# Kernel tuning notes

Hardware: AMD Instinct MI355X
Metric: run time of the kernel (lower is better)

## Reference

```python
import jax, jax.numpy as jnp
import numpy as np

GROUPS = 32
EPS = 1e-6


def group_norm(x, gamma, beta):
    # x: [B, C, T], normalize per group of channels over (C//G, T)
    B, C, T = x.shape
    xr = x.reshape(B, GROUPS, C // GROUPS, T)
    mean = xr.mean(axis=(2, 3), keepdims=True)
    var = xr.var(axis=(2, 3), keepdims=True)
    xn = ((xr - mean) * jax.lax.rsqrt(var + EPS)).reshape(B, C, T)
    return xn * gamma[None, :, None] + beta[None, :, None]


def conv1x1(h, w, b):
    # 1x1 Conv1d == channel matmul. h: [B,C,T], w: [O,C], b: [O]
    return jnp.einsum('oc,bct->bot', w, h) + b[None, :, None]


def setup_inputs() -> dict:
    key = jax.random.key(0)
    ks = jax.random.split(key, 10)
    B, C, T = 8, 512, 2048
    s = 1.0 / np.sqrt(C)
    return {
        'x': jax.random.normal(ks[0], (B, C, T), jnp.float32),
        'gamma': jnp.ones((C,), jnp.float32),
        'beta': jnp.zeros((C,), jnp.float32),
        'q_w': jax.random.normal(ks[1], (C, C), jnp.float32) * s,
        'q_b': jnp.zeros((C,), jnp.float32),
        'k_w': jax.random.normal(ks[2], (C, C), jnp.float32) * s,
        'k_b': jnp.zeros((C,), jnp.float32),
        'v_w': jax.random.normal(ks[3], (C, C), jnp.float32) * s,
        'v_b': jnp.zeros((C,), jnp.float32),
        'o_w': jax.random.normal(ks[4], (C, C), jnp.float32) * s,
        'o_b': jnp.zeros((C,), jnp.float32),
    }


def reference(x, gamma, beta, q_w, q_b, k_w, k_b, v_w, v_b, o_w, o_b):
    h = group_norm(x, gamma, beta)
    q = conv1x1(h, q_w, q_b)  # [B,C,T]
    k = conv1x1(h, k_w, k_b)
    v = conv1x1(h, v_w, v_b)
    B, C, T = q.shape
    scale = jnp.asarray(C, q.dtype) ** -0.5
    # scores[b,t,s] = sum_c q[b,c,t] * k[b,c,s]
    scores = jnp.einsum('bct,bcs->bts', q, k) * scale
    w = jax.nn.softmax(scores, axis=-1)
    # out[b,c,t] = sum_s v[b,c,s] * w[b,t,s]
    h = jnp.einsum('bcs,bts->bct', v, w)
    h = conv1x1(h, o_w, o_b)
    return x + h
```

## Files before the change

kernel.cpp:

```cpp
#include <hip/hip_runtime.h>
#include <hip/hip_bf16.h>
#include <stdint.h>

typedef __bf16 bf16_t;
typedef __attribute__((ext_vector_type(8))) __bf16 bf16x8;
typedef __attribute__((ext_vector_type(4))) __bf16 bf16x4;
typedef __attribute__((ext_vector_type(4))) float f32x4;

__device__ __forceinline__ bool is_fp32(const void* gamma) {
  return ((const unsigned*)gamma)[0] == 0x3F800000u;
}

__device__ __forceinline__ void async_copy16(const bf16_t* g, bf16_t* l) {
  __builtin_amdgcn_global_load_lds(
      (const __attribute__((address_space(1))) void*)g,
      (__attribute__((address_space(3))) void*)l, 16, 0, 0);
}

#define GFENCE() asm volatile("" ::: "memory")

__device__ __forceinline__ void hard_barrier() {
  GFENCE();
  __builtin_amdgcn_sched_barrier(0);
  __builtin_amdgcn_s_barrier();
  __builtin_amdgcn_sched_barrier(0);
  GFENCE();
}

template <int NW>
__device__ __forceinline__ void vm_wait() {
  if constexpr (NW == 8)
    asm volatile("s_waitcnt vmcnt(8)" ::: "memory");
  else if constexpr (NW == 6)
    asm volatile("s_waitcnt vmcnt(6)" ::: "memory");
  else if constexpr (NW == 3)
    asm volatile("s_waitcnt vmcnt(3)" ::: "memory");
  else
    asm volatile("s_waitcnt vmcnt(0)" ::: "memory");
}

__global__ __launch_bounds__(512) void gnorm(
    const void* __restrict__ xv, const void* __restrict__ gamma,
    const void* __restrict__ beta, const void* __restrict__ q_w,
    const void* __restrict__ k_w, const void* __restrict__ v_w,
    const void* __restrict__ o_w, const void* __restrict__ q_b,
    const void* __restrict__ k_b, const void* __restrict__ v_b,
    const void* __restrict__ o_b, bf16_t* __restrict__ wdst,
    float* __restrict__ rowsum, bf16_t* __restrict__ ht) {
  const bool fp32 = is_fp32(gamma);
  const int bid = blockIdx.x;
  const int tid = threadIdx.x;
  if (bid < 64) {
    const void* wsrc[4] = {q_w, k_w, v_w, o_w};
#pragma unroll
    for (int r = 0; r < 4; ++r) {
      int e = (bid * 2048 + r * 512 + tid) * 8;
      int seg = e >> 18, off = e & 262143;
      const void* s = wsrc[seg];
      bf16x8 w8;
      if (fp32) {
        const float* sf = (const float*)s + off;
        float4 u = *(const float4*)sf;
        float4 w = *(const float4*)(sf + 4);
        w8[0] = (bf16_t)u.x; w8[1] = (bf16_t)u.y;
        w8[2] = (bf16_t)u.z; w8[3] = (bf16_t)u.w;
        w8[4] = (bf16_t)w.x; w8[5] = (bf16_t)w.y;
        w8[6] = (bf16_t)w.z; w8[7] = (bf16_t)w.w;
      } else {
        w8 = *(const bf16x8*)((const bf16_t*)s + off);
      }
      *(bf16x8*)(wdst + e) = w8;
    }
    if (bid == 0) {
      bf16_t* vdst = wdst + 4 * 262144;
      const void* vsrc[6] = {gamma, beta, q_b, k_b, v_b, o_b};
#pragma unroll
      for (int rep = 0; rep < 6; ++rep) {
        const void* s2 = vsrc[rep];
        vdst[rep * 512 + tid] = fp32 ? (bf16_t)((const float*)s2)[tid]
                                     : ((const bf16_t*)s2)[tid];
      }
    }
    if (bid >= 1 && bid <= 8) {
      float4 z = {0.f, 0.f, 0.f, 0.f};
      *(float4*)(rowsum + (((bid - 1) << 9) + tid) * 4) = z;
    }
    return;
  }
  __shared__ float tile[16 * 2052];
  __shared__ float red[16];
  const int gn = bid - 64;
  const int b = gn >> 5, g = gn & 31;
  const long long base = ((long long)b * 512 + g * 16) * 2048;
  float s1 = 0.f, s2 = 0.f;
  if (fp32) {
    const float* xf = (const float*)xv + base;
#pragma unroll
    for (int p = 0; p < 16; ++p) {
      float4 u = *(const float4*)(xf + p * 2048 + tid * 4);
      s1 += u.x + u.y + u.z + u.w;
      s2 += u.x * u.x + u.y * u.y + u.z * u.z + u.w * u.w;
      *(float4*)&tile[p * 2052 + tid * 4] = u;
    }
  } else {
    const bf16_t* xb = (const bf16_t*)xv + base;
#pragma unroll
    for (int p = 0; p < 16; ++p) {
      bf16x4 v4 = *(const bf16x4*)(xb + p * 2048 + tid * 4);
      float4 u;
      u.x = (float)v4[0]; u.y = (float)v4[1];
      u.z = (float)v4[2]; u.w = (float)v4[3];
      s1 += u.x + u.y + u.z + u.w;
      s2 += u.x * u.x + u.y * u.y + u.z * u.z + u.w * u.w;
      *(float4*)&tile[p * 2052 + tid * 4] = u;
    }
  }
  for (int o = 32; o > 0; o >>= 1) {
    s1 += __shfl_down(s1, o);
    s2 += __shfl_down(s2, o);
  }
  const int wv = tid >> 6, ln = tid & 63;
  if (ln == 0) { red[wv] = s1; red[8 + wv] = s2; }
  __syncthreads();
  float a = 0.f, c2 = 0.f;
#pragma unroll
  for (int w = 0; w < 8; ++w) { a += red[w]; c2 += red[8 + w]; }
  const float inv = 1.0f / 32768.0f;
  float mean = a * inv;
  float var = c2 * inv - mean * mean;
  float rstd = rsqrtf(var + 1e-6f);

  const int c = ln & 15;
  const int tq = ln >> 4;
  const int gc = g * 16 + c;
  float gamv = fp32 ? ((const float*)gamma)[gc]
                    : (float)((const bf16_t*)gamma)[gc];
  float betv = fp32 ? ((const float*)beta)[gc]
                    : (float)((const bf16_t*)beta)[gc];
  float sc = rstd * gamv;
  float sh = betv - mean * sc;
  bf16_t* hb = ht + (long long)b * 2048 * 512 + g * 16;
#pragma unroll 4
  for (int pass = 0; pass < 64; ++pass) {
    int t = wv * 256 + pass * 4 + tq;
    float v = tile[c * 2052 + t];
    hb[(long long)t * 512 + c] = (bf16_t)(v * sc + sh);
  }
}

template <bool BIASM, bool BIASN, bool EXPSUM, int M, int N, int K, int LDA,
          int LDB, int LDC>
__device__ __forceinline__ void gemm_ring3(
    const bf16_t* __restrict__ A, long long sA, const bf16_t* __restrict__ B,
    long long sB, bf16_t* __restrict__ Cout, long long sC,
    const bf16_t* __restrict__ biasM, const bf16_t* __restrict__ biasN,
    float alpha, float* __restrict__ rowsum, int m0, int n0, int b,
    bf16_t* lds) {
  const int tid = threadIdx.x;
  const int lane = tid & 63;
  const int lane15 = lane & 15;
  const int quad = lane >> 4;
  const int wave = tid >> 6;
  const int wm = wave >> 2;
  const int wn = wave & 3;

  bf16_t* ldsA = lds;
  bf16_t* ldsB = lds + 3 * 4096;

  const int srow = tid >> 2;
  const int sg = ((tid & 3) - (srow >> 1)) & 3;
  const long long B128 = 128LL * LDB;
  const bf16_t* As_src = A + (long long)b * sA + (long long)m0 * LDA +
                         (long long)srow * LDA + sg * 8;
  const bf16_t* Bs_src = B + (long long)b * sB + (long long)n0 * LDB +
                         (long long)srow * LDB + sg * 8;

  auto stA = [&](int kelem, int r) {
    async_copy16(As_src + kelem, ldsA + r * 4096 + tid * 8);
  };
  auto stB = [&](int kelem, int r) {
    async_copy16(Bs_src + kelem, ldsB + r * 8192 + tid * 8);
    async_copy16(Bs_src + B128 + kelem, ldsB + r * 8192 + tid * 8 + 4096);
  };

  const int slot = ((quad + (lane15 >> 1)) & 3) * 8;
  const int aoff = (wm * 64 + lane15) * 32 + slot;
  const int boff = (wn * 64 + lane15) * 32 + slot;

  bf16x8 af[4];
  f32x4 acc[4][4];
#pragma unroll
  for (int i = 0; i < 4; ++i)
#pragma unroll
    for (int j = 0; j < 4; ++j) acc[i][j] = {0.f, 0.f, 0.f, 0.f};

  auto ldbf = [&](int r, int j) {
    return *(const bf16x8*)(ldsB + r * 8192 + boff + j * 512);
  };

  constexpr int NT = K / 32;

  stA(0, 0); stB(0, 0);
  stA(32, 1); stB(32, 1);
  vm_wait<3>();
  hard_barrier();

#pragma unroll 1
  for (int kt = 0; kt < NT; ++kt) {
    const int rd = kt % 3;
    const int rs = (kt + 2) % 3;
    const int ks = ((kt + 2) % NT) * 32;
#pragma unroll
    for (int i = 0; i < 4; ++i)
      af[i] = *(const bf16x8*)(ldsA + rd * 4096 + aoff + i * 512);
    bf16x8 b0 = ldbf(rd, 0), b1 = ldbf(rd, 1);
    stA(ks, rs);
    hard_barrier();
    asm volatile("s_waitcnt lgkmcnt(0)" ::: "memory");
    __builtin_amdgcn_sched_barrier(0);
    __builtin_amdgcn_s_setprio(1);
#pragma unroll
    for (int i = 0; i < 4; ++i) {
      acc[i][0] = __builtin_amdgcn_mfma_f32_16x16x32_bf16(af[i], b0, acc[i][0], 0, 0, 0);
      acc[i][1] = __builtin_amdgcn_mfma_f32_16x16x32_bf16(af[i], b1, acc[i][1], 0, 0, 0);
    }
    __builtin_amdgcn_s_setprio(0);
    hard_barrier();
    bf16x8 b2 = ldbf(rd, 2), b3 = ldbf(rd, 3);
    stB(ks, rs);
    hard_barrier();
    asm volatile("s_waitcnt lgkmcnt(0)" ::: "memory");
    __builtin_amdgcn_sched_barrier(0);
    __builtin_amdgcn_s_setprio(1);
#pragma unroll
    for (int i = 0; i < 4; ++i) {
      acc[i][2] = __builtin_amdgcn_mfma_f32_16x16x32_bf16(af[i], b2, acc[i][2], 0, 0, 0);
      acc[i][3] = __builtin_amdgcn_mfma_f32_16x16x32_bf16(af[i], b3, acc[i][3], 0, 0, 0);
    }
    __builtin_amdgcn_s_setprio(0);
    vm_wait<3>();
    hard_barrier();
  }
  asm volatile("s_waitcnt vmcnt(0)" ::: "memory");
  hard_barrier();

  bf16_t* ebuf = lds;
  if constexpr (EXPSUM) {
#pragma unroll
    for (int i = 0; i < 4; ++i) {
#pragma unroll
      for (int r = 0; r < 4; ++r) {
        int ml = wm * 64 + i * 16 + quad * 4 + r;
        float partial = 0.f;
#pragma unroll
        for (int j = 0; j < 4; ++j) {
          int nl = wn * 64 + j * 16 + lane15;
          float v = __expf(acc[i][j][r] * alpha);
          partial += v;
          ebuf[(ml * 256 + nl) ^ ((ml & 7) << 3)] = (bf16_t)v;
        }
        partial += __shfl_xor(partial, 1);
        partial += __shfl_xor(partial, 2);
        partial += __shfl_xor(partial, 4);
        partial += __shfl_xor(partial, 8);
        if (lane15 == 0)
          atomicAdd(&rowsum[(long long)b * M + m0 + ml], partial);
      }
    }
  } else {
#pragma unroll
    for (int i = 0; i < 4; ++i) {
#pragma unroll
      for (int j = 0; j < 4; ++j) {
#pragma unroll
        for (int r = 0; r < 4; ++r) {
          int ml = wm * 64 + i * 16 + quad * 4 + r;
          int nl = wn * 64 + j * 16 + lane15;
          float v = acc[i][j][r] * alpha;
          if constexpr (BIASM) v += (float)biasM[m0 + ml];
          if constexpr (BIASN) v += (float)biasN[n0 + nl];
          ebuf[(ml * 256 + nl) ^ ((ml & 7) << 3)] = (bf16_t)v;
        }
      }
    }
  }
  __syncthreads();
  bf16_t* Co = Cout + (long long)b * sC;
#pragma unroll
  for (int p = 0; p < 8; ++p) {
    int v8 = tid + p * 512;
    int mr = v8 >> 5, c8 = v8 & 31;
    bf16x8 w = *(const bf16x8*)&ebuf[(mr * 256 + c8 * 8) ^ ((mr & 7) << 3)];
    *(bf16x8*)&Co[(long long)(m0 + mr) * LDC + n0 + c8 * 8] = w;
  }
}

template <int BM, bool BIASM, bool BIASN, bool RESOUT, bool EXPSUM,
          bool NORMROW, int M, int N, int K, int LDA, int LDB, int LDC>
__device__ __forceinline__ void gemm8_body(
    const bf16_t* __restrict__ A, long long sA, const bf16_t* __restrict__ B,
    long long sB, void* __restrict__ Cout, long long sC,
    const bf16_t* __restrict__ biasM, const bf16_t* __restrict__ biasN,
    const void* __restrict__ Res, long long sR, float alpha,
    const void* __restrict__ gamma, float* __restrict__ rowsum, int m0,
    int n0, int b, bf16_t* lds) {
  static_assert(!RESOUT || BM == 128, "RESOUT epilogue assumes BM=128");
  constexpr int AI = BM / 32;
  constexpr int AR = BM * 32;
  constexpr int L = BM / 128 + 2;
  const int tid = threadIdx.x;
  const int lane = tid & 63;
  const int lane15 = lane & 15;
  const int quad = lane >> 4;
  const int wave = tid >> 6;
  const int wm = wave >> 2;
  const int wn = wave & 3;

  bf16_t* ldsA = lds;
  bf16_t* ldsB = lds + 4 * AR;

  const int srow = tid >> 2;
  const int sg = ((tid & 3) - (srow >> 1)) & 3;
  const long long A128 = 128LL * LDA, B128 = 128LL * LDB;
  const bf16_t* As_src = A + (long long)b * sA + (long long)m0 * LDA +
                         (long long)srow * LDA + sg * 8;
  const bf16_t* Bs_src = B + (long long)b * sB + (long long)n0 * LDB +
                         (long long)srow * LDB + sg * 8;

  auto stA = [&](int kelem, int r) {
    async_copy16(As_src + kelem, ldsA + r * AR + tid * 8);
    if constexpr (BM == 256)
      async_copy16(As_src + A128 + kelem, ldsA + r * AR + tid * 8 + 4096);
  };
  auto stB = [&](int kelem, int r) {
    async_copy16(Bs_src + kelem, ldsB + r * 8192 + tid * 8);
    async_copy16(Bs_src + B128 + kelem, ldsB + r * 8192 + tid * 8 + 4096);
  };

  const int slot = ((quad + (lane15 >> 1)) & 3) * 8;
  const int aoff = (wm * (BM / 2) + lane15) * 32 + slot;
  const int boff = (wn * 64 + lane15) * 32 + slot;

  bf16x8 af[AI];
  f32x4 acc[AI][4];
#pragma unroll
  for (int i = 0; i < AI; ++i)
#pragma unroll
    for (int j = 0; j < 4; ++j) acc[i][j] = {0.f, 0.f, 0.f, 0.f};

  auto lda_frags = [&](int r) {
#pragma unroll
    for (int i = 0; i < AI; ++i)
      af[i] = *(const bf16x8*)(ldsA + r * AR + aoff + i * 512);
  };
  auto ldbf = [&](int r, int j) {
    return *(const bf16x8*)(ldsB + r * 8192 + boff + j * 512);
  };

  auto phaseA = [&](int rdA, int rdB, int stk, int str) {
    lda_frags(rdA);
    bf16x8 b0 = ldbf(rdB, 0), b1 = ldbf(rdB, 1);
    stA(stk, str);
    hard_barrier();
    asm volatile("s_waitcnt lgkmcnt(0)" ::: "memory");
    __builtin_amdgcn_sched_barrier(0);
    __builtin_amdgcn_s_setprio(1);
#pragma unroll
    for (int i = 0; i < AI; ++i) {
      acc[i][0] = __builtin_amdgcn_mfma_f32_16x16x32_bf16(af[i], b0, acc[i][0], 0, 0, 0);
      acc[i][1] = __builtin_amdgcn_mfma_f32_16x16x32_bf16(af[i], b1, acc[i][1], 0, 0, 0);
    }
    __builtin_amdgcn_s_setprio(0);
    hard_barrier();
  };
  auto phaseB = [&](int rdB, int stk, int str) {
    bf16x8 b0 = ldbf(rdB, 2), b1 = ldbf(rdB, 3);
    stB(stk, str);
    hard_barrier();
    asm volatile("s_waitcnt lgkmcnt(0)" ::: "memory");
    __builtin_amdgcn_sched_barrier(0);
    __builtin_amdgcn_s_setprio(1);
#pragma unroll
    for (int i = 0; i < AI; ++i) {
      acc[i][2] = __builtin_amdgcn_mfma_f32_16x16x32_bf16(af[i], b0, acc[i][2], 0, 0, 0);
      acc[i][3] = __builtin_amdgcn_mfma_f32_16x16x32_bf16(af[i], b1, acc[i][3], 0, 0, 0);
    }
    __builtin_amdgcn_s_setprio(0);
    vm_wait<2 * L>();
    hard_barrier();
  };

  constexpr int NI = K / 128;

  stA(0, 0); stB(0, 0);
  stA(32, 1); stB(32, 1);
  stA(64, 2); stB(64, 2);
  vm_wait<2 * L>();
  hard_barrier();

#pragma unroll 1
  for (int it = 0; it < NI; ++it) {
    const int ku = it * 128;
    const bool lastit = (it == NI - 1);
    const int k0n = lastit ? 0 : ku + 128;
    const int k1n = lastit ? 32 : ku + 160;
    const int k2n = lastit ? 64 : ku + 192;
    phaseA(0, 0, ku + 96, 3);
    phaseB(0, ku + 96, 3);
    phaseA(1, 1, k0n, 0);
    phaseB(1, k0n, 0);
    phaseA(2, 2, k1n, 1);
    phaseB(2, k1n, 1);
    phaseA(3, 3, k2n, 2);
    phaseB(3, k2n, 2);
  }
  asm volatile("s_waitcnt vmcnt(0)" ::: "memory");
  hard_barrier();

  if constexpr (RESOUT) {
    float* fbuf = (float*)lds;
#pragma unroll
    for (int i = 0; i < AI; ++i) {
#pragma unroll
      for (int j = 0; j < 4; ++j) {
#pragma unroll
        for (int r = 0; r < 4; ++r) {
          int ml = wm * (BM / 2) + i * 16 + quad * 4 + r;
          int nl = wn * 64 + j * 16 + lane15;
          float v = acc[i][j][r] * alpha;
          if constexpr (BIASM) v += (float)biasM[m0 + ml];
          if constexpr (BIASN) v += (float)biasN[n0 + nl];
          fbuf[(ml * 256 + nl) ^ ((ml & 7) << 2)] = v;
        }
      }
    }
    __syncthreads();
    const bool f32o = is_fp32(gamma);
#pragma unroll
    for (int p = 0; p < BM / 8; ++p) {
      int v4 = tid + p * 512;
      int mr = v4 >> 6, c4 = v4 & 63;
      float4 w = *(const float4*)&fbuf[(mr * 256 + c4 * 4) ^ ((mr & 7) << 2)];
      long long base = (long long)(m0 + mr) * LDC + n0 + c4 * 4;
      if (f32o) {
        float4 xr = *(const float4*)((const float*)Res + (long long)b * sR + base);
        w.x += xr.x; w.y += xr.y; w.z += xr.z; w.w += xr.w;
        *(float4*)&((float*)Cout)[(long long)b * sC + base] = w;
      } else {
        bf16x4 xr = *(const bf16x4*)((const bf16_t*)Res + (long long)b * sR + base);
        bf16x4 o4;
        o4[0] = (bf16_t)(w.x + (float)xr[0]);
        o4[1] = (bf16_t)(w.y + (float)xr[1]);
        o4[2] = (bf16_t)(w.z + (float)xr[2]);
        o4[3] = (bf16_t)(w.w + (float)xr[3]);
        *(bf16x4*)&((bf16_t*)Cout)[(long long)b * sC + base] = o4;
      }
    }
    return;
  }

  {
    float invr[AI][4];
    if constexpr (NORMROW) {
#pragma unroll
      for (int i = 0; i < AI; ++i)
#pragma unroll
        for (int r = 0; r < 4; ++r)
          invr[i][r] = 1.0f / rowsum[(long long)b * M + m0 + wm * (BM / 2) +
                                     i * 16 + quad * 4 + r];
    }
    bf16_t* ebuf = lds;
#pragma unroll
    for (int i = 0; i < AI; ++i) {
#pragma unroll
      for (int j = 0; j < 4; ++j) {
#pragma unroll
        for (int r = 0; r < 4; ++r) {
          int ml = wm * (BM / 2) + i * 16 + quad * 4 + r;
          int nl = wn * 64 + j * 16 + lane15;
          float v = acc[i][j][r] * alpha;
          if constexpr (NORMROW) v *= invr[i][r];
          if constexpr (BIASM) v += (float)biasM[m0 + ml];
          if constexpr (BIASN) v += (float)biasN[n0 + nl];
          ebuf[(ml * 256 + nl) ^ ((ml & 7) << 3)] = (bf16_t)v;
        }
      }
    }
    __syncthreads();
    bf16_t* Co = (bf16_t*)Cout + (long long)b * sC;
#pragma unroll
    for (int p = 0; p < BM / 16; ++p) {
      int v8 = tid + p * 512;
      int mr = v8 >> 5, c8 = v8 & 31;
      bf16x8 w = *(const bf16x8*)&ebuf[(mr * 256 + c8 * 8) ^ ((mr & 7) << 3)];
      *(bf16x8*)&Co[(long long)(m0 + mr) * LDC + n0 + c8 * 8] = w;
    }
  }
}

__global__ __launch_bounds__(512, 4) void qkv_fat(
    const bf16_t* __restrict__ ht, const bf16_t* __restrict__ wdst,
    bf16_t* __restrict__ qkt, bf16_t* __restrict__ vvb,
    const void* __restrict__ gamma) {
  __shared__ __align__(16) bf16_t lds[36864];
  const long long TC = 2048LL * 512, CT = 512LL * 2048;
  const bf16_t* vdst = wdst + 4 * 262144;
  const bf16_t* qkb = vdst + 1024;
  const bf16_t* vbb = vdst + 2048;
  const bf16_t* wv = wdst + 2 * 262144;
  int bid = blockIdx.x;
  if (bid < 512) {
    int b = bid >> 6, rem = bid & 63;
    int m0 = (rem >> 2) * 128, n0 = (rem & 3) * 256;
    gemm_ring3<false, true, false, 2048, 1024, 512, 512, 512, 1024>(
        ht, TC, wdst, 0, qkt, 2048LL * 1024, nullptr, qkb, 1.0f, nullptr, m0,
        n0, b, lds);
  } else {
    int id2 = bid - 512;
    int b = id2 >> 5, rem = id2 & 31;
    int m0 = (rem & 3) * 128, n0 = (rem >> 2) * 256;
    gemm_ring3<true, false, false, 512, 2048, 512, 512, 512, 2048>(
        wv, 0, ht, TC, vvb, CT, vbb, nullptr, 1.0f, nullptr, m0, n0, b, lds);
  }
}

__global__ __launch_bounds__(512, 4) void scores_kernel(
    const bf16_t* __restrict__ qkt, bf16_t* __restrict__ Sm,
    const void* __restrict__ gamma, float* __restrict__ rowsum, float alpha) {
  __shared__ __align__(16) bf16_t lds[36864];
  int x = blockIdx.x;
  int gid = x >> 4, win = x & 15;
  int gm = gid & 3, gn = gid >> 2;
  int m0 = (gm * 4 + (win & 3)) * 128;
  int n0 = (gn * 4 + (win >> 2)) * 256;
  gemm_ring3<false, false, true, 2048, 2048, 512, 1024, 1024, 2048>(
      qkt, 2048LL * 1024, qkt + 512, 2048LL * 1024, Sm, 2048LL * 2048,
      nullptr, nullptr, alpha, rowsum, m0, n0, blockIdx.z, lds);
}

__global__ __launch_bounds__(512, 2) void av_kernel(
    const bf16_t* __restrict__ Sm, const bf16_t* __restrict__ vvb,
    bf16_t* __restrict__ h2t, const void* __restrict__ gamma,
    float* __restrict__ rowsum) {
  __shared__ __align__(16) bf16_t lds[49152];
  gemm8_body<128, false, false, false, false, true, 2048, 512, 2048, 2048,
             2048, 512>(Sm, 2048LL * 2048, vvb, 512LL * 2048, h2t,
                        2048LL * 512, nullptr, nullptr, nullptr, 0, 1.0f,
                        gamma, rowsum, blockIdx.y * 128, blockIdx.x * 256,
                        blockIdx.z, lds);
}

__global__ __launch_bounds__(512, 2) void final_kernel(
    const bf16_t* __restrict__ wdst, const bf16_t* __restrict__ h2t,
    void* __restrict__ out, const void* __restrict__ x,
    const void* __restrict__ gamma) {
  __shared__ __align__(16) bf16_t lds[65536];
  const bf16_t* vdst = wdst + 4 * 262144;
  const bf16_t* obb = vdst + 2560;
  const bf16_t* wo = wdst + 3 * 262144;
  gemm8_body<128, true, false, true, false, false, 512, 2048, 512, 512, 512,
             2048>(wo, 0, h2t, 2048LL * 512, out, 512LL * 2048, obb, nullptr,
                   x, 512LL * 2048, 1.0f, gamma, nullptr, blockIdx.y * 128,
                   blockIdx.x * 256, blockIdx.z, lds);
}

extern "C" void kernel_launch(void* const* d_in, const int* in_sizes, int n_in,
                              void* d_out, int out_size, void* d_ws,
                              size_t ws_size, hipStream_t stream) {
  const void* x = d_in[0];
  const void* gamma = d_in[1];
  const void* beta = d_in[2];
  const void* q_w = d_in[3];
  const void* q_b = d_in[4];
  const void* k_w = d_in[5];
  const void* k_b = d_in[6];
  const void* v_w = d_in[7];
  const void* v_b = d_in[8];
  const void* o_w = d_in[9];
  const void* o_b = d_in[10];

  const long long BTC = 8LL * 2048 * 512;
  char* ws = (char*)d_ws;
  bf16_t* wdst = (bf16_t*)(ws + 4096);
  float* rowsum = (float*)(ws + 4096 + 2 * 1024 * 1024 + 8192);
  const size_t hdr = 4096 + 2 * 1024 * 1024 + 8192 + 65536;
  bf16_t* ht = (bf16_t*)(ws + hdr);
  bf16_t* vvb = ht + BTC;
  bf16_t* Sm = vvb + BTC;
  bf16_t* qkt = (bf16_t*)d_out;

  const float scale = 0.044194173824159216f;

  gnorm<<<320, 512, 0, stream>>>(x, gamma, beta, q_w, k_w, v_w, o_w, q_b, k_b,
                                 v_b, o_b, wdst, rowsum, ht);
  qkv_fat<<<768, 512, 0, stream>>>(ht, wdst, qkt, vvb, gamma);
  scores_kernel<<<dim3(128, 1, 8), 512, 0, stream>>>(qkt, Sm, gamma, rowsum,
                                                     scale);
  av_kernel<<<dim3(2, 16, 8), 512, 0, stream>>>(Sm, vvb, ht, gamma, rowsum);
  final_kernel<<<dim3(8, 4, 8), 512, 0, stream>>>(wdst, ht, d_out, x, gamma);
}
```

Baseline: 266.9 us.

## Generalize ring3 GEMM to BN=128 and use it for V projection and AV

Templates the three-stage ring GEMM on tile width BN, merges the two half-K-step phases into one stage/compute step with fewer barriers, and adds a row-normalization epilogue. The V projection and the attention-times-V kernel switch to 128x128 tiles with more blocks and higher occupancy (AV now uses the ring GEMM with 4 blocks/CU and smaller LDS). This aims to improve load balance and latency hiding, though smaller tiles lower data reuse per block and merging the phases changes the overlap between loads and MFMA.

```diff
diff --git a/kernel.cpp b/kernel.cpp
--- a/kernel.cpp
+++ b/kernel.cpp
@@ -35,6 +35,8 @@
     asm volatile("s_waitcnt vmcnt(6)" ::: "memory");
   else if constexpr (NW == 3)
     asm volatile("s_waitcnt vmcnt(3)" ::: "memory");
+  else if constexpr (NW == 2)
+    asm volatile("s_waitcnt vmcnt(2)" ::: "memory");
   else
     asm volatile("s_waitcnt vmcnt(0)" ::: "memory");
 }
@@ -148,14 +150,17 @@
   }
 }
 
-template <bool BIASM, bool BIASN, bool EXPSUM, int M, int N, int K, int LDA,
-          int LDB, int LDC>
+template <int BN, bool BIASM, bool BIASN, bool EXPSUM, bool NORMROW, int M,
+          int N, int K, int LDA, int LDB, int LDC>
 __device__ __forceinline__ void gemm_ring3(
     const bf16_t* __restrict__ A, long long sA, const bf16_t* __restrict__ B,
     long long sB, bf16_t* __restrict__ Cout, long long sC,
     const bf16_t* __restrict__ biasM, const bf16_t* __restrict__ biasN,
     float alpha, float* __restrict__ rowsum, int m0, int n0, int b,
     bf16_t* lds) {
+  constexpr int BJ = BN / 64;
+  constexpr int BR = BN * 32;
+  constexpr int L = 1 + BN / 128;
   const int tid = threadIdx.x;
   const int lane = tid & 63;
   const int lane15 = lane & 15;
@@ -175,34 +180,29 @@
   const bf16_t* Bs_src = B + (long long)b * sB + (long long)n0 * LDB +
                          (long long)srow * LDB + sg * 8;
 
-  auto stA = [&](int kelem, int r) {
+  auto stage = [&](int kelem, int r) {
     async_copy16(As_src + kelem, ldsA + r * 4096 + tid * 8);
-  };
-  auto stB = [&](int kelem, int r) {
-    async_copy16(Bs_src + kelem, ldsB + r * 8192 + tid * 8);
-    async_copy16(Bs_src + B128 + kelem, ldsB + r * 8192 + tid * 8 + 4096);
+    async_copy16(Bs_src + kelem, ldsB + r * BR + tid * 8);
+    if constexpr (BN == 256)
+      async_copy16(Bs_src + B128 + kelem, ldsB + r * BR + tid * 8 + 4096);
   };
 
   const int slot = ((quad + (lane15 >> 1)) & 3) * 8;
   const int aoff = (wm * 64 + lane15) * 32 + slot;
-  const int boff = (wn * 64 + lane15) * 32 + slot;
-
-  bf16x8 af[4];
-  f32x4 acc[4][4];
+  const int boff = (wn * (BN / 4) + lane15) * 32 + slot;
+
+  bf16x8 af[4], bfr[BJ];
+  f32x4 acc[4][BJ];
 #pragma unroll
   for (int i = 0; i < 4; ++i)
 #pragma unroll
-    for (int j = 0; j < 4; ++j) acc[i][j] = {0.f, 0.f, 0.f, 0.f};
-
-  auto ldbf = [&](int r, int j) {
-    return *(const bf16x8*)(ldsB + r * 8192 + boff + j * 512);
-  };
+    for (int j = 0; j < BJ; ++j) acc[i][j] = {0.f, 0.f, 0.f, 0.f};
 
   constexpr int NT = K / 32;
 
-  stA(0, 0); stB(0, 0);
-  stA(32, 1); stB(32, 1);
-  vm_wait<3>();
+  stage(0, 0);
+  stage(32, 1);
+  vm_wait<L>();
   hard_barrier();
 
 #pragma unroll 1
@@ -213,32 +213,21 @@
 #pragma unroll
     for (int i = 0; i < 4; ++i)
       af[i] = *(const bf16x8*)(ldsA + rd * 4096 + aoff + i * 512);
-    bf16x8 b0 = ldbf(rd, 0), b1 = ldbf(rd, 1);
-    stA(ks, rs);
-    hard_barrier();
+#pragma unroll
+    for (int j = 0; j < BJ; ++j)
+      bfr[j] = *(const bf16x8*)(ldsB + rd * BR + boff + j * 512);
+    stage(ks, rs);
     asm volatile("s_waitcnt lgkmcnt(0)" ::: "memory");
     __builtin_amdgcn_sched_barrier(0);
     __builtin_amdgcn_s_setprio(1);
 #pragma unroll
-    for (int i = 0; i < 4; ++i) {
-      acc[i][0] = __builtin_amdgcn_mfma_f32_16x16x32_bf16(af[i], b0, acc[i][0], 0, 0, 0);
-      acc[i][1] = __builtin_amdgcn_mfma_f32_16x16x32_bf16(af[i], b1, acc[i][1], 0, 0, 0);
-    }
+    for (int i = 0; i < 4; ++i)
+#pragma unroll
+      for (int j = 0; j < BJ; ++j)
+        acc[i][j] = __builtin_amdgcn_mfma_f32_16x16x32_bf16(af[i], bfr[j],
+                                                            acc[i][j], 0, 0, 0);
     __builtin_amdgcn_s_setprio(0);
-    hard_barrier();
-    bf16x8 b2 = ldbf(rd, 2), b3 = ldbf(rd, 3);
-    stB(ks, rs);
-    hard_barrier();
-    asm volatile("s_waitcnt lgkmcnt(0)" ::: "memory");
-    __builtin_amdgcn_sched_barrier(0);
-    __builtin_amdgcn_s_setprio(1);
-#pragma unroll
-    for (int i = 0; i < 4; ++i) {
-      acc[i][2] = __builtin_amdgcn_mfma_f32_16x16x32_bf16(af[i], b2, acc[i][2], 0, 0, 0);
-      acc[i][3] = __builtin_amdgcn_mfma_f32_16x16x32_bf16(af[i], b3, acc[i][3], 0, 0, 0);
-    }
-    __builtin_amdgcn_s_setprio(0);
-    vm_wait<3>();
+    vm_wait<L>();
     hard_barrier();
   }
   asm volatile("s_waitcnt vmcnt(0)" ::: "memory");
@@ -253,11 +242,11 @@
         int ml = wm * 64 + i * 16 + quad * 4 + r;
         float partial = 0.f;
 #pragma unroll
-        for (int j = 0; j < 4; ++j) {
-          int nl = wn * 64 + j * 16 + lane15;
+        for (int j = 0; j < BJ; ++j) {
+          int nl = wn * (BN / 4) + j * 16 + lane15;
           float v = __expf(acc[i][j][r] * alpha);
           partial += v;
-          ebuf[(ml * 256 + nl) ^ ((ml & 7) << 3)] = (bf16_t)v;
+          ebuf[(ml * BN + nl) ^ ((ml & 7) << 3)] = (bf16_t)v;
         }
         partial += __shfl_xor(partial, 1);
         partial += __shfl_xor(partial, 2);
@@ -268,29 +257,40 @@
       }
     }
   } else {
+    float invr[4][4];
+    if constexpr (NORMROW) {
+#pragma unroll
+      for (int i = 0; i < 4; ++i)
+#pragma unroll
+        for (int r = 0; r < 4; ++r)
+          invr[i][r] = 1.0f / rowsum[(long long)b * M + m0 + wm * 64 + i * 16 +
+                                     quad * 4 + r];
+    }
 #pragma unroll
     for (int i = 0; i < 4; ++i) {
 #pragma unroll
-      for (int j = 0; j < 4; ++j) {
+      for (int j = 0; j < BJ; ++j) {
 #pragma unroll
         for (int r = 0; r < 4; ++r) {
           int ml = wm * 64 + i * 16 + quad * 4 + r;
-          int nl = wn * 64 + j * 16 + lane15;
+          int nl = wn * (BN / 4) + j * 16 + lane15;
           float v = acc[i][j][r] * alpha;
+          if constexpr (NORMROW) v *= invr[i][r];
           if constexpr (BIASM) v += (float)biasM[m0 + ml];
           if constexpr (BIASN) v += (float)biasN[n0 + nl];
-          ebuf[(ml * 256 + nl) ^ ((ml & 7) << 3)] = (bf16_t)v;
+          ebuf[(ml * BN + nl) ^ ((ml & 7) << 3)] = (bf16_t)v;
         }
       }
     }
   }
   __syncthreads();
   bf16_t* Co = Cout + (long long)b * sC;
-#pragma unroll
-  for (int p = 0; p < 8; ++p) {
+  constexpr int GPR = BN / 8;
+#pragma unroll
+  for (int p = 0; p < (128 * BN) / 4096; ++p) {
     int v8 = tid + p * 512;
-    int mr = v8 >> 5, c8 = v8 & 31;
-    bf16x8 w = *(const bf16x8*)&ebuf[(mr * 256 + c8 * 8) ^ ((mr & 7) << 3)];
+    int mr = v8 / GPR, c8 = v8 % GPR;
+    bf16x8 w = *(const bf16x8*)&ebuf[(mr * BN + c8 * 8) ^ ((mr & 7) << 3)];
     *(bf16x8*)&Co[(long long)(m0 + mr) * LDC + n0 + c8 * 8] = w;
   }
 }
@@ -304,7 +304,6 @@
     const void* __restrict__ Res, long long sR, float alpha,
     const void* __restrict__ gamma, float* __restrict__ rowsum, int m0,
     int n0, int b, bf16_t* lds) {
-  static_assert(!RESOUT || BM == 128, "RESOUT epilogue assumes BM=128");
   constexpr int AI = BM / 32;
   constexpr int AR = BM * 32;
   constexpr int L = BM / 128 + 2;
@@ -512,15 +511,16 @@
   if (bid < 512) {
     int b = bid >> 6, rem = bid & 63;
     int m0 = (rem >> 2) * 128, n0 = (rem & 3) * 256;
-    gemm_ring3<false, true, false, 2048, 1024, 512, 512, 512, 1024>(
-        ht, TC, wdst, 0, qkt, 2048LL * 1024, nullptr, qkb, 1.0f, nullptr, m0,
-        n0, b, lds);
+    gemm_ring3<256, false, true, false, false, 2048, 1024, 512, 512, 512,
+               1024>(ht, TC, wdst, 0, qkt, 2048LL * 1024, nullptr, qkb, 1.0f,
+                     nullptr, m0, n0, b, lds);
   } else {
     int id2 = bid - 512;
-    int b = id2 >> 5, rem = id2 & 31;
-    int m0 = (rem & 3) * 128, n0 = (rem >> 2) * 256;
-    gemm_ring3<true, false, false, 512, 2048, 512, 512, 512, 2048>(
-        wv, 0, ht, TC, vvb, CT, vbb, nullptr, 1.0f, nullptr, m0, n0, b, lds);
+    int b = id2 >> 6, rem = id2 & 63;
+    int m0 = (rem & 3) * 128, n0 = (rem >> 2) * 128;
+    gemm_ring3<128, true, false, false, false, 512, 2048, 512, 512, 512,
+               2048>(wv, 0, ht, TC, vvb, CT, vbb, nullptr, 1.0f, nullptr, m0,
+                     n0, b, lds);
   }
 }
 
@@ -533,21 +533,23 @@
   int gm = gid & 3, gn = gid >> 2;
   int m0 = (gm * 4 + (win & 3)) * 128;
   int n0 = (gn * 4 + (win >> 2)) * 256;
-  gemm_ring3<false, false, true, 2048, 2048, 512, 1024, 1024, 2048>(
-      qkt, 2048LL * 1024, qkt + 512, 2048LL * 1024, Sm, 2048LL * 2048,
-      nullptr, nullptr, alpha, rowsum, m0, n0, blockIdx.z, lds);
-}
-
-__global__ __launch_bounds__(512, 2) void av_kernel(
+  gemm_ring3<256, false, false, true, false, 2048, 2048, 512, 1024, 1024,
+             2048>(qkt, 2048LL * 1024, qkt + 512, 2048LL * 1024, Sm,
+                   2048LL * 2048, nullptr, nullptr, alpha, rowsum, m0, n0,
+                   blockIdx.z, lds);
+}
+
+__global__ __launch_bounds__(512, 4) void av_kernel(
     const bf16_t* __restrict__ Sm, const bf16_t* __restrict__ vvb,
     bf16_t* __restrict__ h2t, const void* __restrict__ gamma,
     float* __restrict__ rowsum) {
-  __shared__ __align__(16) bf16_t lds[49152];
-  gemm8_body<128, false, false, false, false, true, 2048, 512, 2048, 2048,
-             2048, 512>(Sm, 2048LL * 2048, vvb, 512LL * 2048, h2t,
-                        2048LL * 512, nullptr, nullptr, nullptr, 0, 1.0f,
-                        gamma, rowsum, blockIdx.y * 128, blockIdx.x * 256,
-                        blockIdx.z, lds);
+  __shared__ __align__(16) bf16_t lds[24576];
+  int bid = blockIdx.x;
+  int b = bid >> 6, rem = bid & 63;
+  int m0 = (rem >> 2) * 128, n0 = (rem & 3) * 128;
+  gemm_ring3<128, false, false, false, true, 2048, 512, 2048, 2048, 2048,
+             512>(Sm, 2048LL * 2048, vvb, 512LL * 2048, h2t, 2048LL * 512,
+                  nullptr, nullptr, 1.0f, rowsum, m0, n0, b, lds);
 }
 
 __global__ __launch_bounds__(512, 2) void final_kernel(
@@ -593,9 +595,9 @@
 
   gnorm<<<320, 512, 0, stream>>>(x, gamma, beta, q_w, k_w, v_w, o_w, q_b, k_b,
                                  v_b, o_b, wdst, rowsum, ht);
-  qkv_fat<<<768, 512, 0, stream>>>(ht, wdst, qkt, vvb, gamma);
+  qkv_fat<<<1024, 512, 0, stream>>>(ht, wdst, qkt, vvb, gamma);
   scores_kernel<<<dim3(128, 1, 8), 512, 0, stream>>>(qkt, Sm, gamma, rowsum,
                                                      scale);
-  av_kernel<<<dim3(2, 16, 8), 512, 0, stream>>>(Sm, vvb, ht, gamma, rowsum);
+  av_kernel<<<512, 512, 0, stream>>>(Sm, vvb, ht, gamma, rowsum);
   final_kernel<<<dim3(8, 4, 8), 512, 0, stream>>>(wdst, ht, d_out, x, gamma);
 }
```

Result: slower. 275.1 us (+3.1%).
